# Kernel optimization log

Hardware: AMD Instinct MI355X
Metric: run time of the kernel (lower is better)

## Reference

```python
import jax, jax.numpy as jnp
import numpy as np

D = 1024  # input_size == context_size

def setup_inputs() -> dict:
    key = jax.random.key(0)
    ks = jax.random.split(key, 8)
    B, S = 16, 4096
    s = 1.0 / np.sqrt(D)
    return {
        "x": jax.random.normal(ks[0], (B, S, D), dtype=jnp.float32),
        "context": jax.random.normal(ks[1], (B, D), dtype=jnp.float32),
        "W_in": jax.random.uniform(ks[2], (D, D), jnp.float32, -s, s),
        "b_in": jax.random.uniform(ks[3], (D,), jnp.float32, -s, s),
        "W_ctx": jax.random.uniform(ks[4], (D, D), jnp.float32, -s, s),
        "b_ctx": jax.random.uniform(ks[5], (D,), jnp.float32, -s, s),
        "w_att": jax.random.uniform(ks[6], (D,), jnp.float32, -s, s),
        "b_att": jax.random.uniform(ks[7], (), jnp.float32, -s, s),
    }

def reference(x, context, W_in, b_in, W_ctx, b_ctx, w_att, b_att):
    # projected_input: [B,S,D]; projected_context: [B,D] broadcast over S
    pi = jnp.einsum('bsd,ed->bse', x, W_in) + b_in
    pc = jnp.einsum('bd,ed->be', context, W_ctx) + b_ctx
    h = jnp.tanh(pi + pc[:, None, :])                      # [B,S,D]
    scores = jnp.einsum('bsd,d->bs', h, w_att) + b_att      # [B,S]
    weights = jax.nn.softmax(scores, axis=1)                # [B,S]
    context_vector = jnp.einsum('bs,bsd->bd', weights, x)   # [B,D]
    # dropout is identity in eval mode
    return context_vector
```

## Files before the change

kernel.cpp:

```cpp
#include <hip/hip_runtime.h>
#include <hip/hip_bf16.h>
#include <math.h>

#define NB 16
#define NS 4096
#define ND 1024
#define NM (NB * NS)

#define WS_T       0
#define WS_SCORES  16384
#define WS_WEIGHTS (WS_SCORES + NB * NS)
#define WS_SHARED  (WS_WEIGHTS + NB * NS)
#define WS_XBF16   (WS_SHARED + 524288)
#define WS_SPART   (WS_XBF16 + 33554432)
#define WS_NEED    (((size_t)WS_SPART + 524288) * 4)

typedef short v8s __attribute__((ext_vector_type(8)));
typedef float v4f __attribute__((ext_vector_type(4)));
typedef unsigned short ushort;

#define G_AS __attribute__((address_space(1)))
#define L_AS __attribute__((address_space(3)))

__device__ __forceinline__ ushort f2bf(float f) {
    __hip_bfloat16 h = __float2bfloat16(f);
    return *reinterpret_cast<ushort*>(&h);
}

__device__ __forceinline__ float bf2f(ushort u) {
    return __uint_as_float(((unsigned)u) << 16);
}

__device__ __forceinline__ float fast_tanh(float x) {
    float e = __expf(2.0f * x);
    return 1.0f - 2.0f / (e + 1.0f);
}

__global__ __launch_bounds__(256) void convw_kernel(const float* __restrict__ W,
                                                    ushort* __restrict__ Wb) {
    int flat = blockIdx.x * 256 + threadIdx.x;
#pragma unroll
    for (int j = 0; j < 2; ++j) {
        int idx = flat + j * 131072;
        float4 v = ((const float4*)W)[idx];
        ushort4 o;
        o.x = f2bf(v.x); o.y = f2bf(v.y); o.z = f2bf(v.z); o.w = f2bf(v.w);
        ((ushort4*)Wb)[idx] = o;
    }
}

__global__ __launch_bounds__(256) void convx_kernel(const float* __restrict__ x,
                                                    ushort* __restrict__ xb) {
    size_t base = (size_t)blockIdx.x * 256 + threadIdx.x;
#pragma unroll
    for (int i = 0; i < 16; ++i) {
        size_t idx8 = base + (size_t)i * 524288;
        float4 a = ((const float4*)x)[idx8 * 2];
        float4 c = ((const float4*)x)[idx8 * 2 + 1];
        v8s o;
        o[0] = (short)f2bf(a.x); o[1] = (short)f2bf(a.y);
        o[2] = (short)f2bf(a.z); o[3] = (short)f2bf(a.w);
        o[4] = (short)f2bf(c.x); o[5] = (short)f2bf(c.y);
        o[6] = (short)f2bf(c.z); o[7] = (short)f2bf(c.w);
        ((v8s*)xb)[idx8] = o;
    }
}

__global__ __launch_bounds__(256) void tvec_kernel(const float* __restrict__ context,
                                                   const float* __restrict__ W_ctx,
                                                   const float* __restrict__ b_in,
                                                   const float* __restrict__ b_ctx,
                                                   float* __restrict__ t) {
    __shared__ float ctx[ND];
    int b = blockIdx.y;
    int tid = threadIdx.x;
    for (int i = tid; i < ND; i += 256) ctx[i] = context[b * ND + i];
    __syncthreads();
    int e = blockIdx.x * 64 + (tid >> 2);
    int kq = tid & 3;
    const float4* wr = (const float4*)(W_ctx + (size_t)e * ND + kq * 256);
    const float4* cr = (const float4*)(ctx + kq * 256);
    float acc = 0.f;
#pragma unroll 4
    for (int k = 0; k < 64; ++k) {
        float4 w = wr[k];
        float4 c = cr[k];
        acc += c.x * w.x + c.y * w.y + c.z * w.z + c.w * w.w;
    }
    acc += __shfl_xor(acc, 1);
    acc += __shfl_xor(acc, 2);
    if (kq == 0) t[b * ND + e] = acc + b_in[e] + b_ctx[e];
}

__global__ __launch_bounds__(256) void scores_tile_kernel(const ushort* __restrict__ xbf,
                                                          const ushort* __restrict__ Wb,
                                                          const float* __restrict__ t,
                                                          const float* __restrict__ w_att,
                                                          float* __restrict__ spart) {
    __shared__ ushort As[3][4096];
    __shared__ ushort Bs[3][4096];
    __shared__ float red[4][64];

    int tid = threadIdx.x;
    int o = blockIdx.x;
    int rt = (o & 7) * 64 + (o >> 6);
    int ct = (o >> 3) & 7;
    int row0 = rt << 7;
    int e0 = ct << 7;
    int b = row0 >> 12;

    int g0 = tid, g1 = tid + 256;
    const ushort* gaA0 = xbf + (size_t)(row0 + (g0 >> 2)) * ND + (g0 & 3) * 8;
    const ushort* gaA1 = xbf + (size_t)(row0 + (g1 >> 2)) * ND + (g1 & 3) * 8;
    const ushort* gaB0 = Wb  + (size_t)(e0  + (g0 >> 2)) * ND + (g0 & 3) * 8;
    const ushort* gaB1 = Wb  + (size_t)(e0  + (g1 >> 2)) * ND + (g1 & 3) * 8;

    int w = tid >> 6, l = tid & 63;
    int l15 = l & 15, kq4 = l >> 4;
    int R = (w >> 1) * 64;
    int E = (w & 1) * 64;

    v4f acc[4][4];
#pragma unroll
    for (int i = 0; i < 4; ++i)
#pragma unroll
        for (int j = 0; j < 4; ++j) acc[i][j] = (v4f)(0.f);

#define STAGE(BUF, KO)                                                                                              \
    {                                                                                                               \
        __builtin_amdgcn_global_load_lds((const G_AS void*)(gaA0 + (KO)), (L_AS void*)&As[BUF][g0 * 8], 16, 0, 0);  \
        __builtin_amdgcn_global_load_lds((const G_AS void*)(gaA1 + (KO)), (L_AS void*)&As[BUF][g1 * 8], 16, 0, 0);  \
        __builtin_amdgcn_global_load_lds((const G_AS void*)(gaB0 + (KO)), (L_AS void*)&Bs[BUF][g0 * 8], 16, 0, 0);  \
        __builtin_amdgcn_global_load_lds((const G_AS void*)(gaB1 + (KO)), (L_AS void*)&Bs[BUF][g1 * 8], 16, 0, 0);  \
    }

#define COMPUTE(BUF)                                                                          \
    {                                                                                         \
        v8s af[4], bf[4];                                                                     \
        _Pragma("unroll") for (int mf = 0; mf < 4; ++mf)                                      \
            af[mf] = *(const v8s*)&As[BUF][((R + mf * 16 + l15) * 4 + kq4) * 8];              \
        _Pragma("unroll") for (int nf = 0; nf < 4; ++nf)                                      \
            bf[nf] = *(const v8s*)&Bs[BUF][((E + nf * 16 + l15) * 4 + kq4) * 8];              \
        _Pragma("unroll") for (int mf = 0; mf < 4; ++mf)                                      \
            _Pragma("unroll") for (int nf = 0; nf < 4; ++nf)                                  \
                acc[mf][nf] = __builtin_amdgcn_mfma_f32_16x16x32_bf16(af[mf], bf[nf],         \
                                                                      acc[mf][nf], 0, 0, 0);  \
    }

#define KSTEP(KT, BUF, STBUF, VMTOK)                                 \
    {                                                                \
        __builtin_amdgcn_s_barrier();                                \
        STAGE(STBUF, ((KT) + 2) * 32);                               \
        asm volatile("s_waitcnt vmcnt(" VMTOK ")" ::: "memory");     \
        __builtin_amdgcn_s_barrier();                                \
        asm volatile("" ::: "memory");                               \
        COMPUTE(BUF);                                                \
    }

    STAGE(0, 0);
    STAGE(1, 32);

    for (int tt = 0; tt < 10; ++tt) {
        KSTEP(3 * tt + 0, 0, 2, "8");
        KSTEP(3 * tt + 1, 1, 0, "8");
        KSTEP(3 * tt + 2, 2, 1, "8");
    }
    __builtin_amdgcn_s_barrier();
    asm volatile("s_waitcnt vmcnt(4)" ::: "memory");
    __builtin_amdgcn_s_barrier();
    asm volatile("" ::: "memory");
    COMPUTE(0);
    __builtin_amdgcn_s_barrier();
    asm volatile("s_waitcnt vmcnt(0)" ::: "memory");
    __builtin_amdgcn_s_barrier();
    asm volatile("" ::: "memory");
    COMPUTE(1);

#undef KSTEP
#undef COMPUTE
#undef STAGE

    float s[4][4];
#pragma unroll
    for (int i = 0; i < 4; ++i)
#pragma unroll
        for (int j = 0; j < 4; ++j) s[i][j] = 0.f;

#pragma unroll
    for (int nf = 0; nf < 4; ++nf) {
        int e = e0 + E + nf * 16 + l15;
        float tv = t[b * ND + e];
        float wv = w_att[e];
#pragma unroll
        for (int mf = 0; mf < 4; ++mf)
#pragma unroll
            for (int r = 0; r < 4; ++r)
                s[mf][r] += fast_tanh(acc[mf][nf][r] + tv) * wv;
    }
#pragma unroll
    for (int mf = 0; mf < 4; ++mf)
#pragma unroll
        for (int r = 0; r < 4; ++r) {
            float v = s[mf][r];
            v += __shfl_xor(v, 1);
            v += __shfl_xor(v, 2);
            v += __shfl_xor(v, 4);
            v += __shfl_xor(v, 8);
            s[mf][r] = v;
        }
    if (l15 == 0) {
#pragma unroll
        for (int mf = 0; mf < 4; ++mf)
#pragma unroll
            for (int r = 0; r < 4; ++r)
                red[w][mf * 16 + kq4 * 4 + r] = s[mf][r];
    }
    __syncthreads();
    if (tid < 128) {
        int half = tid >> 6;
        int rl = tid & 63;
        float v = red[half * 2][rl] + red[half * 2 + 1][rl];
        spart[ct * 65536 + row0 + half * 64 + rl] = v;
    }
}

__global__ __launch_bounds__(512) void scores_mfma_kernel(const float* __restrict__ x,
                                                          const ushort* __restrict__ Wb,
                                                          const float* __restrict__ t,
                                                          const float* __restrict__ w_att,
                                                          float* __restrict__ scores) {
    __shared__ ushort As[2][64 * 256];
    __shared__ float red[8][64];

    int tid = threadIdx.x;
    int row0 = blockIdx.x * 64;
    int b = row0 >> 12;
    const float4* xf4 = (const float4*)x;

    int sr = tid >> 3;
    int sc = tid & 7;
    int swzbase = (sr & 7) << 3;

    float4 nx[8];
#pragma unroll
    for (int j = 0; j < 8; ++j)
        nx[j] = xf4[(size_t)(row0 + sr) * 256 + sc + j * 8];
#pragma unroll
    for (int j = 0; j < 8; ++j) {
        int c4 = sc + j * 8;
        ushort4 o;
        o.x = f2bf(nx[j].x); o.y = f2bf(nx[j].y); o.z = f2bf(nx[j].z); o.w = f2bf(nx[j].w);
        *(ushort4*)&As[0][sr * 256 + ((c4 * 4) ^ swzbase)] = o;
    }
    __syncthreads();

    int w = tid >> 6;
    int l = tid & 63;
    int l15 = l & 15;
    int kofs = (l >> 4) * 8;
    int xorv = (l & 7) << 3;
    int n0 = w * 128;

    v4f acc[2][4][4];
#pragma unroll
    for (int p = 0; p < 2; ++p)
#pragma unroll
        for (int i = 0; i < 4; ++i)
#pragma unroll
            for (int j = 0; j < 4; ++j) acc[p][i][j] = (v4f)(0.f);

    const ushort* bbase0 = Wb + (size_t)(n0 + l15) * ND + kofs;
    const ushort* bbase1 = bbase0 + (size_t)64 * ND;

#pragma unroll
    for (int kh = 0; kh < 4; ++kh) {
        if (kh < 3) {
#pragma unroll
            for (int j = 0; j < 8; ++j)
                nx[j] = xf4[(size_t)(row0 + sr) * 256 + (kh + 1) * 64 + sc + j * 8];
        }
        const ushort* Ab = &As[kh & 1][0];
        int kb = kh * 256;

        v8s b0c[4], b0n[4], b1[4];
#pragma unroll
        for (int nf = 0; nf < 4; ++nf) b0c[nf] = *(const v8s*)(bbase0 + (size_t)nf * 16 * ND + kb);

#pragma unroll
        for (int ks = 0; ks < 8; ++ks) {
            int kk = kb + ks * 32;
            int elem = (ks * 32 + kofs) ^ xorv;
            v8s af[4];
#pragma unroll
            for (int mf = 0; mf < 4; ++mf)
                af[mf] = *(const v8s*)&Ab[(mf * 16 + l15) * 256 + elem];
#pragma unroll
            for (int nf = 0; nf < 4; ++nf)
                b1[nf] = *(const v8s*)(bbase1 + (size_t)nf * 16 * ND + kk);
            if (ks < 7) {
#pragma unroll
                for (int nf = 0; nf < 4; ++nf)
                    b0n[nf] = *(const v8s*)(bbase0 + (size_t)nf * 16 * ND + kk + 32);
            }
#pragma unroll
            for (int mf = 0; mf < 4; ++mf)
#pragma unroll
                for (int nf = 0; nf < 4; ++nf)
                    acc[0][mf][nf] = __builtin_amdgcn_mfma_f32_16x16x32_bf16(
                        af[mf], b0c[nf], acc[0][mf][nf], 0, 0, 0);
#pragma unroll
            for (int mf = 0; mf < 4; ++mf)
#pragma unroll
                for (int nf = 0; nf < 4; ++nf)
                    acc[1][mf][nf] = __builtin_amdgcn_mfma_f32_16x16x32_bf16(
                        af[mf], b1[nf], acc[1][mf][nf], 0, 0, 0);
#pragma unroll
            for (int nf = 0; nf < 4; ++nf) b0c[nf] = b0n[nf];
        }

        if (kh < 3) {
#pragma unroll
            for (int j = 0; j < 8; ++j) {
                int c4 = sc + j * 8;
                ushort4 o;
                o.x = f2bf(nx[j].x); o.y = f2bf(nx[j].y); o.z = f2bf(nx[j].z); o.w = f2bf(nx[j].w);
                *(ushort4*)&As[(kh + 1) & 1][sr * 256 + ((c4 * 4) ^ swzbase)] = o;
            }
            __syncthreads();
        }
    }

    float s[4][4];
#pragma unroll
    for (int i = 0; i < 4; ++i)
#pragma unroll
        for (int j = 0; j < 4; ++j) s[i][j] = 0.f;

#pragma unroll
    for (int pass = 0; pass < 2; ++pass)
#pragma unroll
        for (int nf = 0; nf < 4; ++nf) {
            int e = n0 + pass * 64 + nf * 16 + l15;
            float tv = t[b * ND + e];
            float wv = w_att[e];
#pragma unroll
            for (int mf = 0; mf < 4; ++mf)
#pragma unroll
                for (int r = 0; r < 4; ++r)
                    s[mf][r] += fast_tanh(acc[pass][mf][nf][r] + tv) * wv;
        }

#pragma unroll
    for (int mf = 0; mf < 4; ++mf)
#pragma unroll
        for (int r = 0; r < 4; ++r) {
            float v = s[mf][r];
            v += __shfl_xor(v, 1);
            v += __shfl_xor(v, 2);
            v += __shfl_xor(v, 4);
            v += __shfl_xor(v, 8);
            s[mf][r] = v;
        }
    if (l15 == 0) {
#pragma unroll
        for (int mf = 0; mf < 4; ++mf)
#pragma unroll
            for (int r = 0; r < 4; ++r)
                red[w][mf * 16 + (l >> 4) * 4 + r] = s[mf][r];
    }
    __syncthreads();
    if (tid < 64) {
        float v = 0.f;
#pragma unroll
        for (int ww = 0; ww < 8; ++ww) v += red[ww][tid];
        scores[(size_t)b * NS + (row0 & (NS - 1)) + tid] = v;
    }
}

__global__ __launch_bounds__(256) void softmax8_kernel(const float* __restrict__ spart,
                                                       float* __restrict__ weights) {
    int b = blockIdx.x;
    int tid = threadIdx.x;
    float v[16];
    float lmax = -1e30f;
#pragma unroll
    for (int i = 0; i < 16; ++i) {
        int grow = b * NS + tid + i * 256;
        float sum = 0.f;
#pragma unroll
        for (int c = 0; c < 8; ++c) sum += spart[c * 65536 + grow];
        v[i] = sum;
        lmax = fmaxf(lmax, sum);
    }
#pragma unroll
    for (int off = 32; off >= 1; off >>= 1) lmax = fmaxf(lmax, __shfl_xor(lmax, off));
    __shared__ float redm[4];
    int wave = tid >> 6;
    if ((tid & 63) == 0) redm[wave] = lmax;
    __syncthreads();
    float bmax = fmaxf(fmaxf(redm[0], redm[1]), fmaxf(redm[2], redm[3]));

    float lsum = 0.f;
#pragma unroll
    for (int i = 0; i < 16; ++i) {
        v[i] = expf(v[i] - bmax);
        lsum += v[i];
    }
#pragma unroll
    for (int off = 32; off >= 1; off >>= 1) lsum += __shfl_xor(lsum, off);
    __shared__ float reds[4];
    if ((tid & 63) == 0) reds[wave] = lsum;
    __syncthreads();
    float inv = 1.0f / (reds[0] + reds[1] + reds[2] + reds[3]);
#pragma unroll
    for (int i = 0; i < 16; ++i) weights[b * NS + tid + i * 256] = v[i] * inv;
}

__global__ __launch_bounds__(256) void softmax_kernel(const float* __restrict__ scores,
                                                      float* __restrict__ weights) {
    int b = blockIdx.x;
    int tid = threadIdx.x;
    float v[16];
    float lmax = -1e30f;
#pragma unroll
    for (int i = 0; i < 16; ++i) {
        v[i] = scores[b * NS + tid + i * 256];
        lmax = fmaxf(lmax, v[i]);
    }
#pragma unroll
    for (int off = 32; off >= 1; off >>= 1) lmax = fmaxf(lmax, __shfl_xor(lmax, off));
    __shared__ float redm[4];
    int wave = tid >> 6;
    if ((tid & 63) == 0) redm[wave] = lmax;
    __syncthreads();
    float bmax = fmaxf(fmaxf(redm[0], redm[1]), fmaxf(redm[2], redm[3]));

    float lsum = 0.f;
#pragma unroll
    for (int i = 0; i < 16; ++i) {
        v[i] = expf(v[i] - bmax);
        lsum += v[i];
    }
#pragma unroll
    for (int off = 32; off >= 1; off >>= 1) lsum += __shfl_xor(lsum, off);
    __shared__ float reds[4];
    if ((tid & 63) == 0) reds[wave] = lsum;
    __syncthreads();
    float inv = 1.0f / (reds[0] + reds[1] + reds[2] + reds[3]);
#pragma unroll
    for (int i = 0; i < 16; ++i) weights[b * NS + tid + i * 256] = v[i] * inv;
}

__global__ __launch_bounds__(256) void wsum_kernel(const float* __restrict__ x,
                                                   const float* __restrict__ w,
                                                   float* __restrict__ part) {
    int sc = blockIdx.x, b = blockIdx.y;
    int d0 = threadIdx.x * 4;
    const float* xb = x + ((size_t)b * NS + sc * 128) * ND;
    const float* wb = w + b * NS + sc * 128;
    float4 acc = {0.f, 0.f, 0.f, 0.f};
    for (int ss = 0; ss < 128; ++ss) {
        float wv = wb[ss];
        float4 xv = *(const float4*)&xb[(size_t)ss * ND + d0];
        acc.x += wv * xv.x;
        acc.y += wv * xv.y;
        acc.z += wv * xv.z;
        acc.w += wv * xv.w;
    }
    *(float4*)&part[(size_t)(b * 32 + sc) * ND + d0] = acc;
}

__global__ __launch_bounds__(256) void wsum_bf_kernel(const ushort* __restrict__ xbf,
                                                      const float* __restrict__ w,
                                                      float* __restrict__ part) {
    int sc = blockIdx.x, b = blockIdx.y;
    int d0 = threadIdx.x * 4;
    const ushort* xb = xbf + ((size_t)b * NS + sc * 128) * ND;
    const float* wb = w + b * NS + sc * 128;
    float4 acc = {0.f, 0.f, 0.f, 0.f};
    for (int ss = 0; ss < 128; ++ss) {
        float wv = wb[ss];
        ushort4 xv = *(const ushort4*)&xb[(size_t)ss * ND + d0];
        acc.x += wv * bf2f(xv.x);
        acc.y += wv * bf2f(xv.y);
        acc.z += wv * bf2f(xv.z);
        acc.w += wv * bf2f(xv.w);
    }
    *(float4*)&part[(size_t)(b * 32 + sc) * ND + d0] = acc;
}

__global__ __launch_bounds__(256) void reduce_kernel(const float* __restrict__ part,
                                                     float* __restrict__ out) {
    int b = blockIdx.x;
    int d0 = threadIdx.x * 4;
    float4 acc = {0.f, 0.f, 0.f, 0.f};
#pragma unroll
    for (int sc = 0; sc < 32; ++sc) {
        float4 v = *(const float4*)&part[(size_t)(b * 32 + sc) * ND + d0];
        acc.x += v.x;
        acc.y += v.y;
        acc.z += v.z;
        acc.w += v.w;
    }
    *(float4*)&out[b * ND + d0] = acc;
}

extern "C" void kernel_launch(void* const* d_in, const int* in_sizes, int n_in,
                              void* d_out, int out_size, void* d_ws, size_t ws_size,
                              hipStream_t stream) {
    const float* x       = (const float*)d_in[0];
    const float* context = (const float*)d_in[1];
    const float* W_in    = (const float*)d_in[2];
    const float* b_in    = (const float*)d_in[3];
    const float* W_ctx   = (const float*)d_in[4];
    const float* b_ctx   = (const float*)d_in[5];
    const float* w_att   = (const float*)d_in[6];

    float* ws      = (float*)d_ws;
    float* t       = ws + WS_T;
    float* scores  = ws + WS_SCORES;
    float* weights = ws + WS_WEIGHTS;
    ushort* wbf16  = (ushort*)(ws + WS_SHARED);
    ushort* xbf16  = (ushort*)(ws + WS_XBF16);
    float* spart   = ws + WS_SPART;
    float* partfb  = ws + WS_SHARED;
    float* out     = (float*)d_out;

    bool fast = ws_size >= WS_NEED;

    convw_kernel<<<dim3(512), 256, 0, stream>>>(W_in, wbf16);
    tvec_kernel<<<dim3(16, NB), 256, 0, stream>>>(context, W_ctx, b_in, b_ctx, t);
    if (fast) {
        convx_kernel<<<dim3(2048), 256, 0, stream>>>(x, xbf16);
        scores_tile_kernel<<<dim3(4096), 256, 0, stream>>>(xbf16, wbf16, t, w_att, spart);
        softmax8_kernel<<<dim3(NB), 256, 0, stream>>>(spart, weights);
        wsum_bf_kernel<<<dim3(32, NB), 256, 0, stream>>>(xbf16, weights, spart);
        reduce_kernel<<<dim3(NB), 256, 0, stream>>>(spart, out);
    } else {
        scores_mfma_kernel<<<dim3(NM / 64), 512, 0, stream>>>(x, wbf16, t, w_att, scores);
        softmax_kernel<<<dim3(NB), 256, 0, stream>>>(scores, weights);
        wsum_kernel<<<dim3(32, NB), 256, 0, stream>>>(x, weights, partfb);
        reduce_kernel<<<dim3(NB), 256, 0, stream>>>(partfb, out);
    }
}
```

Before: 319.3 us.

## Enlarge scores GEMM tile to 256x256 with 512-thread blocks

Measured after the change: 282.7 us. 1.13x faster.

```diff
diff --git a/kernel.cpp b/kernel.cpp
--- a/kernel.cpp
+++ b/kernel.cpp
@@ -92,59 +92,62 @@
     if (kq == 0) t[b * ND + e] = acc + b_in[e] + b_ctx[e];
 }
 
-__global__ __launch_bounds__(256) void scores_tile_kernel(const ushort* __restrict__ xbf,
+__global__ __launch_bounds__(512) void scores_tile_kernel(const ushort* __restrict__ xbf,
                                                           const ushort* __restrict__ Wb,
                                                           const float* __restrict__ t,
                                                           const float* __restrict__ w_att,
                                                           float* __restrict__ spart) {
-    __shared__ ushort As[3][4096];
-    __shared__ ushort Bs[3][4096];
-    __shared__ float red[4][64];
+    __shared__ ushort As[3][8192];
+    __shared__ ushort Bs[3][8192];
+    __shared__ float red[8][128];
 
     int tid = threadIdx.x;
     int o = blockIdx.x;
-    int rt = (o & 7) * 64 + (o >> 6);
-    int ct = (o >> 3) & 7;
-    int row0 = rt << 7;
-    int e0 = ct << 7;
+    int xcd = o & 7, idx = o >> 3;
+    int ct = idx & 3;
+    int rt = xcd * 32 + (idx >> 2);
+    int row0 = rt << 8;
+    int e0 = ct << 8;
     int b = row0 >> 12;
 
-    int g0 = tid, g1 = tid + 256;
-    const ushort* gaA0 = xbf + (size_t)(row0 + (g0 >> 2)) * ND + (g0 & 3) * 8;
-    const ushort* gaA1 = xbf + (size_t)(row0 + (g1 >> 2)) * ND + (g1 & 3) * 8;
-    const ushort* gaB0 = Wb  + (size_t)(e0  + (g0 >> 2)) * ND + (g0 & 3) * 8;
-    const ushort* gaB1 = Wb  + (size_t)(e0  + (g1 >> 2)) * ND + (g1 & 3) * 8;
-
-    int w = tid >> 6, l = tid & 63;
+    const ushort* gaA0 = xbf + (size_t)(row0 + (tid >> 2)) * ND + (tid & 3) * 8;
+    const ushort* gaA1 = gaA0 + (size_t)128 * ND;
+    const ushort* gaB0 = Wb + (size_t)(e0 + (tid >> 2)) * ND + (tid & 3) * 8;
+    const ushort* gaB1 = gaB0 + (size_t)128 * ND;
+
+    int wid = tid >> 6, l = tid & 63;
     int l15 = l & 15, kq4 = l >> 4;
-    int R = (w >> 1) * 64;
-    int E = (w & 1) * 64;
-
-    v4f acc[4][4];
-#pragma unroll
-    for (int i = 0; i < 4; ++i)
+    int WM = (wid >> 2) * 128;
+    int WN = (wid & 3) * 64;
+
+    v4f acc[8][4];
+#pragma unroll
+    for (int i = 0; i < 8; ++i)
 #pragma unroll
         for (int j = 0; j < 4; ++j) acc[i][j] = (v4f)(0.f);
 
-#define STAGE(BUF, KO)                                                                                              \
-    {                                                                                                               \
-        __builtin_amdgcn_global_load_lds((const G_AS void*)(gaA0 + (KO)), (L_AS void*)&As[BUF][g0 * 8], 16, 0, 0);  \
-        __builtin_amdgcn_global_load_lds((const G_AS void*)(gaA1 + (KO)), (L_AS void*)&As[BUF][g1 * 8], 16, 0, 0);  \
-        __builtin_amdgcn_global_load_lds((const G_AS void*)(gaB0 + (KO)), (L_AS void*)&Bs[BUF][g0 * 8], 16, 0, 0);  \
-        __builtin_amdgcn_global_load_lds((const G_AS void*)(gaB1 + (KO)), (L_AS void*)&Bs[BUF][g1 * 8], 16, 0, 0);  \
-    }
-
-#define COMPUTE(BUF)                                                                          \
-    {                                                                                         \
-        v8s af[4], bf[4];                                                                     \
-        _Pragma("unroll") for (int mf = 0; mf < 4; ++mf)                                      \
-            af[mf] = *(const v8s*)&As[BUF][((R + mf * 16 + l15) * 4 + kq4) * 8];              \
-        _Pragma("unroll") for (int nf = 0; nf < 4; ++nf)                                      \
-            bf[nf] = *(const v8s*)&Bs[BUF][((E + nf * 16 + l15) * 4 + kq4) * 8];              \
-        _Pragma("unroll") for (int mf = 0; mf < 4; ++mf)                                      \
-            _Pragma("unroll") for (int nf = 0; nf < 4; ++nf)                                  \
-                acc[mf][nf] = __builtin_amdgcn_mfma_f32_16x16x32_bf16(af[mf], bf[nf],         \
-                                                                      acc[mf][nf], 0, 0, 0);  \
+#define STAGE(BUF, KO)                                                                                                 \
+    {                                                                                                                  \
+        __builtin_amdgcn_global_load_lds((const G_AS void*)(gaA0 + (KO)), (L_AS void*)&As[BUF][tid * 8], 16, 0, 0);    \
+        __builtin_amdgcn_global_load_lds((const G_AS void*)(gaA1 + (KO)), (L_AS void*)&As[BUF][(tid + 512) * 8], 16, 0, 0); \
+        __builtin_amdgcn_global_load_lds((const G_AS void*)(gaB0 + (KO)), (L_AS void*)&Bs[BUF][tid * 8], 16, 0, 0);    \
+        __builtin_amdgcn_global_load_lds((const G_AS void*)(gaB1 + (KO)), (L_AS void*)&Bs[BUF][(tid + 512) * 8], 16, 0, 0); \
+    }
+
+#define COMPUTE(BUF)                                                                              \
+    {                                                                                             \
+        v8s bf[4];                                                                                \
+        _Pragma("unroll") for (int nf = 0; nf < 4; ++nf)                                          \
+            bf[nf] = *(const v8s*)&Bs[BUF][((WN + nf * 16 + l15) * 4 + kq4) * 8];                 \
+        _Pragma("unroll") for (int g = 0; g < 2; ++g) {                                           \
+            v8s af[4];                                                                            \
+            _Pragma("unroll") for (int j = 0; j < 4; ++j)                                         \
+                af[j] = *(const v8s*)&As[BUF][((WM + (g * 4 + j) * 16 + l15) * 4 + kq4) * 8];     \
+            _Pragma("unroll") for (int j = 0; j < 4; ++j)                                         \
+                _Pragma("unroll") for (int nf = 0; nf < 4; ++nf)                                  \
+                    acc[g * 4 + j][nf] = __builtin_amdgcn_mfma_f32_16x16x32_bf16(                 \
+                        af[j], bf[nf], acc[g * 4 + j][nf], 0, 0, 0);                              \
+        }                                                                                         \
     }
 
 #define KSTEP(KT, BUF, STBUF, VMTOK)                                 \
@@ -180,25 +183,25 @@
 #undef COMPUTE
 #undef STAGE
 
-    float s[4][4];
-#pragma unroll
-    for (int i = 0; i < 4; ++i)
+    float s[8][4];
+#pragma unroll
+    for (int i = 0; i < 8; ++i)
 #pragma unroll
         for (int j = 0; j < 4; ++j) s[i][j] = 0.f;
 
 #pragma unroll
     for (int nf = 0; nf < 4; ++nf) {
-        int e = e0 + E + nf * 16 + l15;
+        int e = e0 + WN + nf * 16 + l15;
         float tv = t[b * ND + e];
         float wv = w_att[e];
 #pragma unroll
-        for (int mf = 0; mf < 4; ++mf)
+        for (int mf = 0; mf < 8; ++mf)
 #pragma unroll
             for (int r = 0; r < 4; ++r)
                 s[mf][r] += fast_tanh(acc[mf][nf][r] + tv) * wv;
     }
 #pragma unroll
-    for (int mf = 0; mf < 4; ++mf)
+    for (int mf = 0; mf < 8; ++mf)
 #pragma unroll
         for (int r = 0; r < 4; ++r) {
             float v = s[mf][r];
@@ -210,17 +213,18 @@
         }
     if (l15 == 0) {
 #pragma unroll
-        for (int mf = 0; mf < 4; ++mf)
+        for (int mf = 0; mf < 8; ++mf)
 #pragma unroll
             for (int r = 0; r < 4; ++r)
-                red[w][mf * 16 + kq4 * 4 + r] = s[mf][r];
-    }
-    __syncthreads();
-    if (tid < 128) {
-        int half = tid >> 6;
-        int rl = tid & 63;
-        float v = red[half * 2][rl] + red[half * 2 + 1][rl];
-        spart[ct * 65536 + row0 + half * 64 + rl] = v;
+                red[wid][mf * 16 + kq4 * 4 + r] = s[mf][r];
+    }
+    __syncthreads();
+    if (tid < 256) {
+        int mg = tid >> 7;
+        int rl = tid & 127;
+        float v = red[mg * 4 + 0][rl] + red[mg * 4 + 1][rl] +
+                  red[mg * 4 + 2][rl] + red[mg * 4 + 3][rl];
+        spart[ct * 65536 + row0 + mg * 128 + rl] = v;
     }
 }
 
@@ -377,7 +381,7 @@
     }
 }
 
-__global__ __launch_bounds__(256) void softmax8_kernel(const float* __restrict__ spart,
+__global__ __launch_bounds__(256) void softmax4_kernel(const float* __restrict__ spart,
                                                        float* __restrict__ weights) {
     int b = blockIdx.x;
     int tid = threadIdx.x;
@@ -388,7 +392,7 @@
         int grow = b * NS + tid + i * 256;
         float sum = 0.f;
 #pragma unroll
-        for (int c = 0; c < 8; ++c) sum += spart[c * 65536 + grow];
+        for (int c = 0; c < 4; ++c) sum += spart[c * 65536 + grow];
         v[i] = sum;
         lmax = fmaxf(lmax, sum);
     }
@@ -532,8 +536,8 @@
     tvec_kernel<<<dim3(16, NB), 256, 0, stream>>>(context, W_ctx, b_in, b_ctx, t);
     if (fast) {
         convx_kernel<<<dim3(2048), 256, 0, stream>>>(x, xbf16);
-        scores_tile_kernel<<<dim3(4096), 256, 0, stream>>>(xbf16, wbf16, t, w_att, spart);
-        softmax8_kernel<<<dim3(NB), 256, 0, stream>>>(spart, weights);
+        scores_tile_kernel<<<dim3(1024), 512, 0, stream>>>(xbf16, wbf16, t, w_att, spart);
+        softmax4_kernel<<<dim3(NB), 256, 0, stream>>>(spart, weights);
         wsum_bf_kernel<<<dim3(32, NB), 256, 0, stream>>>(xbf16, weights, spart);
         reduce_kernel<<<dim3(NB), 256, 0, stream>>>(spart, out);
     } else {
```
